# Kernel optimization log

Hardware: AMD Instinct MI355X
Metric: run time of the kernel (lower is better)

The kernel has to match this reference:

```python
import jax, jax.numpy as jnp
import numpy as np

BN_EPS = 1e-4  # KAIR BatchNorm2d eps


def conv1x1(x, W, b):
    # x: (b,c,h,w), W: (out,in), b: (out,)
    return jnp.einsum('oc,bchw->bohw', W, x) + b[None, :, None, None]


def setup_inputs() -> dict:
    key = jax.random.key(0)
    ks = jax.random.split(key, 16)
    b, c, h, w = 8, 64, 128, 128
    f32 = jnp.float32

    def rn(k, shape, s=0.05):
        return jax.random.normal(k, shape, f32) * s

    c3 = 3 * c
    return {
        'x': jax.random.normal(ks[0], (b, c, h, w), f32),
        'xf': jax.random.normal(ks[1], (b, c, h, w), f32),
        'xr': jax.random.normal(ks[2], (b, c, h, w), f32),
        'Wx': rn(ks[3], (c, c)), 'bx': jnp.zeros((c,), f32),
        'Wx1': rn(ks[4], (c, c)), 'bx1': jnp.zeros((c,), f32),
        'Wx2': rn(ks[5], (c, c)), 'bx2': jnp.zeros((c,), f32),
        'Wxf': rn(ks[6], (c, c)), 'bxf': jnp.zeros((c,), f32),
        'Wxr': rn(ks[7], (c, c)), 'bxr': jnp.zeros((c,), f32),
        'W_msa': rn(ks[8], (c3, c3, 3, 3)), 'b_msa': jnp.zeros((c3,), f32),
        'bn_gamma': jnp.ones((c3,), f32), 'bn_beta': jnp.zeros((c3,), f32),
        'bn_mean': jnp.zeros((c3,), f32), 'bn_var': jnp.ones((c3,), f32),
    }


def reference(x, xf, xr, Wx, bx, Wx1, bx1, Wx2, bx2, Wxf, bxf, Wxr, bxr,
              W_msa, b_msa, bn_gamma, bn_beta, bn_mean, bn_var):
    x_org = x
    # 1x1 conv projections (note: x1/x2 are projections of the projected x)
    xp = conv1x1(x, Wx, bx)
    x1 = conv1x1(xp, Wx1, bx1)
    x2 = conv1x1(xp, Wx2, bx2)
    xfp = conv1x1(xf, Wxf, bxf)
    xrp = conv1x1(xr, Wxr, bxr)

    # score1 = rearrange(x1,'b c h w->b h c w') @ rearrange(xf,'b c h w->b h w c') -> (b,h,c,c)
    score1 = jnp.einsum('bchw,bdhw->bhcd', x1, xfp)
    # feature_xf = score1 @ rearrange(x,'b c h w->b h c w'), rearranged back to (b,c,h,w)
    feature_xf = jnp.einsum('bhcd,bdhw->bchw', score1, xp)
    score2 = jnp.einsum('bchw,bdhw->bhcd', x2, xrp)
    feature_xr = jnp.einsum('bhcd,bdhw->bchw', score2, xp)

    out = jnp.concatenate([feature_xf, feature_xr, x_org], axis=1)  # (b,3c,h,w)
    # msa_conv: Conv2d(3c,3c,3,s=1,p=1) + BatchNorm2d(eval) + ReLU
    out = jax.lax.conv_general_dilated(
        out, W_msa, window_strides=(1, 1), padding='SAME',
        dimension_numbers=('NCHW', 'OIHW', 'NCHW'))
    out = out + b_msa[None, :, None, None]
    inv = jax.lax.rsqrt(bn_var + BN_EPS)
    out = (out - bn_mean[None, :, None, None]) * (bn_gamma * inv)[None, :, None, None] \
          + bn_beta[None, :, None, None]
    return jax.nn.relu(out)
```

## Files before the change

### kernel.cpp

```cpp
#include <hip/hip_runtime.h>

#define BATCH 8
#define C     64
#define H     128
#define WD    128
#define C3    192
#define HW    (H*WD)
#define PW    130
#define CBUF  (4*PW*64)

#define SWZ(r) ((((r) & 7) ^ (((r) >> 3) & 6)))

typedef __attribute__((ext_vector_type(8))) short short8;
typedef __attribute__((ext_vector_type(4))) float f32x4;
typedef unsigned short ushort_t;

__device__ __forceinline__ unsigned short f2bf(float f) {
    unsigned u = __builtin_bit_cast(unsigned, f);
    u += 0x7fffu + ((u >> 16) & 1u);
    return (unsigned short)(u >> 16);
}
__device__ __forceinline__ int pack2(unsigned short lo, unsigned short hi) {
    return (int)(((unsigned)hi << 16) | (unsigned)lo);
}

__global__ __launch_bounds__(64) void compose_kernel(
    const float* __restrict__ Wx,  const float* __restrict__ bx,
    const float* __restrict__ Wx1, const float* __restrict__ bx1,
    const float* __restrict__ Wx2, const float* __restrict__ bx2,
    const float* __restrict__ Wxf, const float* __restrict__ bxf,
    const float* __restrict__ Wxr, const float* __restrict__ bxr,
    ushort_t* __restrict__ Wall, float* __restrict__ ball)
{
    int o = blockIdx.x;
    int c = threadIdx.x;
    Wall[0*4096 + o*64 + c] = f2bf(Wx [o*64 + c]);
    Wall[3*4096 + o*64 + c] = f2bf(Wxf[o*64 + c]);
    Wall[4*4096 + o*64 + c] = f2bf(Wxr[o*64 + c]);
    float a1 = 0.f, a2 = 0.f;
    for (int k = 0; k < 64; ++k) {
        float wc = Wx[k*64 + c];
        a1 += Wx1[o*64 + k] * wc;
        a2 += Wx2[o*64 + k] * wc;
    }
    Wall[1*4096 + o*64 + c] = f2bf(a1);
    Wall[2*4096 + o*64 + c] = f2bf(a2);
    float t1 = Wx1[o*64 + c] * bx[c];
    float t2 = Wx2[o*64 + c] * bx[c];
    for (int off = 32; off; off >>= 1) {
        t1 += __shfl_down(t1, off);
        t2 += __shfl_down(t2, off);
    }
    if (c == 0) {
        ball[0*64 + o] = bx[o];
        ball[1*64 + o] = bx1[o] + t1;
        ball[2*64 + o] = bx2[o] + t2;
        ball[3*64 + o] = bxf[o];
        ball[4*64 + o] = bxr[o];
    }
}

__global__ __launch_bounds__(256) void prep_kernel(
    const float* __restrict__ x, const float* __restrict__ xf,
    const float* __restrict__ xr,
    ushort_t* __restrict__ xcl, ushort_t* __restrict__ feat,
    ushort_t* __restrict__ xfT, ushort_t* __restrict__ xrT)
{
    int b  = blockIdx.x / PW, py = blockIdx.x % PW;
    int t  = threadIdx.x;
    const size_t prow = ((size_t)b*PW + py)*PW;

    if (py == 0 || py == PW-1) {
        int4 z = make_int4(0,0,0,0);
        for (int j = t; j < PW*128/8; j += 256) ((int4*)(feat + prow*128))[j] = z;
        for (int j = t; j < PW*64/8;  j += 256) ((int4*)(xcl  + prow*64 ))[j] = z;
        return;
    }
    if (t < 48) {
        int4 z = make_int4(0,0,0,0);
        if (t < 32) {
            int side = t >> 4, seg = t & 15;
            *(int4*)(feat + (prow + (side ? PW-1 : 0))*128 + seg*8) = z;
        } else {
            int u = t - 32, side = u >> 3, seg = u & 7;
            *(int4*)(xcl + (prow + (side ? PW-1 : 0))*64 + seg*8) = z;
        }
    }
    __shared__ ushort_t sx[128*72];
    const int y = py - 1;

    for (int k = t; k < 64*128; k += 256) {
        int c = k >> 7, xx = k & 127;
        sx[xx*72 + c] = f2bf(x[((size_t)b*C + c)*HW + (size_t)y*WD + xx]);
    }
    __syncthreads();
    for (int j = t; j < 128*8; j += 256) {
        int xx = j >> 3, seg = j & 7;
        *(int4*)(xcl + (prow + xx + 1)*64 + seg*8) = *(const int4*)(sx + xx*72 + seg*8);
    }
    __syncthreads();
    for (int k = t; k < 64*128; k += 256) {
        int c = k >> 7, xx = k & 127;
        sx[xx*72 + c] = f2bf(xf[((size_t)b*C + c)*HW + (size_t)y*WD + xx]);
    }
    __syncthreads();
    for (int j = t; j < 128*8; j += 256) {
        int xx = j >> 3, seg = j & 7;
        *(int4*)(xfT + (((size_t)b*128 + y)*128 + xx)*64 + seg*8) = *(const int4*)(sx + xx*72 + seg*8);
    }
    __syncthreads();
    for (int k = t; k < 64*128; k += 256) {
        int c = k >> 7, xx = k & 127;
        sx[xx*72 + c] = f2bf(xr[((size_t)b*C + c)*HW + (size_t)y*WD + xx]);
    }
    __syncthreads();
    for (int j = t; j < 128*8; j += 256) {
        int xx = j >> 3, seg = j & 7;
        *(int4*)(xrT + (((size_t)b*128 + y)*128 + xx)*64 + seg*8) = *(const int4*)(sx + xx*72 + seg*8);
    }
}

__global__ __launch_bounds__(256, 3) void attn_mfma(
    const ushort_t* __restrict__ xcl, const ushort_t* __restrict__ xfT,
    const ushort_t* __restrict__ xrT,
    const ushort_t* __restrict__ Wall, const float* __restrict__ ball,
    ushort_t* __restrict__ feat)
{
    __shared__ ushort_t lds[6*4096];
    ushort_t* P = lds;
    ushort_t* Q = lds + 4096;
    ushort_t* U = lds + 2*4096;
    ushort_t* R = lds + 3*4096;
    ushort_t* V = lds + 4*4096;
    ushort_t* T = lds + 5*4096;

    const int t = threadIdx.x;
    const int wv = t >> 6, lane = t & 63, m = lane & 15, quad = lane >> 4;
    const int b = blockIdx.x >> 7, h = blockIdx.x & 127;
    const size_t rowbase = ((size_t)b*PW + h + 1)*PW;
    const ushort_t* xrow  = xcl + (rowbase + 1)*64;
    const ushort_t* xfrow = xfT + ((size_t)b*128 + h)*128*64;
    const ushort_t* xrrow = xrT + ((size_t)b*128 + h)*128*64;

    auto stageT = [&](const ushort_t* base, ushort_t* dst) {
#pragma unroll
        for (int it = 0; it < 2; ++it) {
            int slot = it*256 + t;
            int w = slot >> 3, seg = slot & 7;
            *(int4*)(dst + w*64 + ((seg ^ SWZ(w)) << 3)) =
                *(const int4*)(base + w*64 + seg*8);
        }
    };
    auto projB = [&](const ushort_t* src, const ushort_t* W, const float* bias,
                     ushort_t* dst) {
        int arow = wv*16 + m;
        int sa = SWZ(arow);
#pragma unroll
        for (int nt = 0; nt < 4; ++nt) {
            f32x4 acc = {0.f,0.f,0.f,0.f};
#pragma unroll
            for (int k = 0; k < 2; ++k) {
                short8 a  = *(const short8*)(src + arow*64 + (((4*k+quad) ^ sa) << 3));
                short8 bb = *(const short8*)(W   + (nt*16 + m)*64  + k*32 + quad*8);
                acc = __builtin_amdgcn_mfma_f32_16x16x32_bf16(a, bb, acc, 0,0,0);
            }
            float bo = bias[nt*16 + m];
            int o = nt*16 + m, w0 = wv*16 + quad*4;
            int base = o*64 + (((w0 >> 3) ^ SWZ(o)) << 3) + (w0 & 7);
            *(int*)(dst + base)     = pack2(f2bf(acc[0]+bo), f2bf(acc[1]+bo));
            *(int*)(dst + base + 2) = pack2(f2bf(acc[2]+bo), f2bf(acc[3]+bo));
        }
    };
    auto projA = [&](const ushort_t* src, const ushort_t* W, const float* bias,
                     ushort_t* dstT) {
        float b4[4];
#pragma unroll
        for (int r = 0; r < 4; ++r) b4[r] = bias[wv*16 + quad*4 + r];
#pragma unroll
        for (int nt = 0; nt < 4; ++nt) {
            f32x4 acc = {0.f,0.f,0.f,0.f};
            int brow = nt*16 + m;
            int sb = SWZ(brow);
#pragma unroll
            for (int k = 0; k < 2; ++k) {
                short8 a  = *(const short8*)(W   + (wv*16 + m)*64  + k*32 + quad*8);
                short8 bb = *(const short8*)(src + brow*64 + (((4*k+quad) ^ sb) << 3));
                acc = __builtin_amdgcn_mfma_f32_16x16x32_bf16(a, bb, acc, 0,0,0);
            }
            int w = nt*16 + m, o0 = wv*16 + quad*4;
            int base = w*64 + (((o0 >> 3) ^ SWZ(w)) << 3) + (o0 & 7);
            *(int*)(dstT + base)     = pack2(f2bf(acc[0]+b4[0]), f2bf(acc[1]+b4[1]));
            *(int*)(dstT + base + 2) = pack2(f2bf(acc[2]+b4[2]), f2bf(acc[3]+b4[3]));
        }
    };
    auto scoreStep = [&](const ushort_t* A, const ushort_t* B, f32x4* sc) {
        int arow = wv*16 + m;
        int sa = SWZ(arow);
#pragma unroll
        for (int nt = 0; nt < 4; ++nt) {
            int brow = nt*16 + m;
            int sb = SWZ(brow);
#pragma unroll
            for (int k = 0; k < 2; ++k) {
                short8 a  = *(const short8*)(A + arow*64 + (((4*k+quad) ^ sa) << 3));
                short8 bb = *(const short8*)(B + brow*64 + (((4*k+quad) ^ sb) << 3));
                sc[nt] = __builtin_amdgcn_mfma_f32_16x16x32_bf16(a, bb, sc[nt], 0,0,0);
            }
        }
    };
    auto scoreDump = [&](const f32x4* sc, ushort_t* dst) {
        int c0 = wv*16 + quad*4;
#pragma unroll
        for (int nt = 0; nt < 4; ++nt) {
            int d = nt*16 + m;
            int gd = d >> 3, dl = d & 7;
#pragma unroll
            for (int r = 0; r < 4; ++r) {
                int row = c0 + r;
                dst[row*64 + ((gd ^ SWZ(row)) << 3) + dl] = f2bf(sc[nt][r]);
            }
        }
    };
    auto featF = [&](const ushort_t* Sc, const ushort_t* XpT, ushort_t* stg) {
        int arow = wv*16 + m;
        int sa = SWZ(arow);
#pragma unroll
        for (int nt = 0; nt < 4; ++nt) {
            f32x4 acc = {0.f,0.f,0.f,0.f};
            int brow = nt*16 + m;
            int sb = SWZ(brow);
#pragma unroll
            for (int k = 0; k < 2; ++k) {
                short8 a  = *(const short8*)(Sc  + arow*64 + (((4*k+quad) ^ sa) << 3));
                short8 bb = *(const short8*)(XpT + brow*64 + (((4*k+quad) ^ sb) << 3));
                acc = __builtin_amdgcn_mfma_f32_16x16x32_bf16(a, bb, acc, 0,0,0);
            }
            int w = nt*16 + m, c0 = wv*16 + quad*4;
            int base = w*64 + (((c0 >> 3) ^ SWZ(w)) << 3) + (c0 & 7);
            *(int*)(stg + base)     = pack2(f2bf(acc[0]), f2bf(acc[1]));
            *(int*)(stg + base + 2) = pack2(f2bf(acc[2]), f2bf(acc[3]));
        }
    };
    auto emitPair = [&](const ushort_t* O1, const ushort_t* O2, int wc) {
#pragma unroll
        for (int it = 0; it < 4; ++it) {
            int j = (it & 1)*256 + t;
            const ushort_t* S = (it < 2) ? O1 : O2;
            int half = (it < 2) ? 0 : 64;
            int row = j >> 3, seg = j & 7;
            int4 v = *(const int4*)(S + row*64 + ((seg ^ SWZ(row)) << 3));
            *(int4*)(feat + (rowbase + wc + 1 + row)*128 + half + seg*8) = v;
        }
    };

    const ushort_t* W0 = Wall;            const float* b0 = ball;
    const ushort_t* W1 = Wall + 4096;     const float* b1 = ball + 64;
    const ushort_t* W2 = Wall + 2*4096;   const float* b2 = ball + 128;
    const ushort_t* W3 = Wall + 3*4096;   const float* b3 = ball + 192;
    const ushort_t* W4 = Wall + 4*4096;   const float* b4 = ball + 256;

    f32x4 sc1[4], sc2[4];
#pragma unroll
    for (int i = 0; i < 4; ++i) { sc1[i] = (f32x4){0,0,0,0}; sc2[i] = (f32x4){0,0,0,0}; }

    stageT(xrow, P); stageT(xfrow, Q); stageT(xrrow, U);
    __syncthreads();
    projB(P, W1, b1, R);  projB(P, W2, b2, V);  projB(Q, W3, b3, T);
    __syncthreads();
    scoreStep(R, T, sc1); projB(U, W4, b4, Q);
    __syncthreads();
    scoreStep(V, Q, sc2);
    stageT(xrow + 64*64, P); stageT(xfrow + 64*64, T); stageT(xrrow + 64*64, U);
    __syncthreads();
    projB(P, W1, b1, R);  projB(P, W2, b2, V);  projB(T, W3, b3, Q);
    __syncthreads();
    scoreStep(R, Q, sc1); projB(U, W4, b4, T);
    __syncthreads();
    scoreStep(V, T, sc2);
    stageT(xrow, P);
    __syncthreads();

    scoreDump(sc1, Q);  scoreDump(sc2, U);
    __syncthreads();
    projA(P, W0, b0, R);
    __syncthreads();
    featF(Q, R, P);  featF(U, R, T);  stageT(xrow + 64*64, V);
    __syncthreads();
    emitPair(P, T, 0);
    __syncthreads();
    projA(V, W0, b0, R);
    __syncthreads();
    featF(Q, R, V);  featF(U, R, T);
    __syncthreads();
    emitPair(V, T, 64);
}

__global__ __launch_bounds__(256) void pack_kernel(const float* __restrict__ W,
                                                   ushort_t* __restrict__ Wpk)
{
    int k = blockIdx.x*256 + threadIdx.x;
    if (k >= 12*54*64) return;
    int lane = k & 63, os = k >> 6;
    int otile = os / 54, s = os % 54;
    int tap = s / 6, icc = s % 6;
    int o   = otile*16 + (lane & 15);
    int ic0 = icc*32 + (lane >> 4)*8;
    ushort_t v[8];
#pragma unroll
    for (int j = 0; j < 8; ++j)
        v[j] = f2bf(W[(size_t)(o*C3 + ic0 + j)*9 + tap]);
    *(int4*)(Wpk + (size_t)k*8) = *(const int4*)v;
}

__global__ __launch_bounds__(512, 2) void conv_mfma(
    const ushort_t* __restrict__ feat, const ushort_t* __restrict__ xcl,
    const ushort_t* __restrict__ Wpk,
    const float* __restrict__ bias, const float* __restrict__ gamma,
    const float* __restrict__ beta, const float* __restrict__ mean,
    const float* __restrict__ var,  float* __restrict__ out)
{
    __shared__ ushort_t sA[2*CBUF];

    const int t = threadIdx.x;
    const int wv = t >> 6, lane = t & 63;
    const int m = lane & 15, quad = lane >> 4;
    const int b  = blockIdx.x >> 6, y0 = (blockIdx.x & 63)*2;
    const int yi = wv & 1, og = wv >> 1;

    f32x4 acc[32];
#pragma unroll
    for (int i = 0; i < 32; ++i) acc[i] = (f32x4){0.f,0.f,0.f,0.f};

    auto produce = [&](int ch, int bufi) {
        ushort_t* dst = sA + bufi*CBUF;
        const ushort_t* base = (ch < 2) ? feat : xcl;
        const int ps = (ch < 2) ? 128 : 64;
        const int co = (ch == 1) ? 64 : 0;
        const int pt = t - 384;
        for (int i = 0; i < 32; ++i) {
            int sl = i*128 + pt;
            int wi = sl & 7, rowgx = sl >> 3;
            int row = rowgx / PW, gx = rowgx - row*PW;
            int wl = wi ^ (gx & 7);
            const ushort_t* g = base + (((size_t)b*PW + y0 + row)*PW + gx)*ps
                                     + co + wl*8;
            __builtin_amdgcn_global_load_lds(
                (const __attribute__((address_space(1))) unsigned int*)g,
                (__attribute__((address_space(3))) unsigned int*)(dst + (size_t)sl*8),
                16, 0, 0);
        }
        if (pt < 64) {
            int sl = 4096 + pt;
            int wi = sl & 7, rowgx = sl >> 3;
            int row = rowgx / PW, gx = rowgx - row*PW;
            int wl = wi ^ (gx & 7);
            const ushort_t* g = base + (((size_t)b*PW + y0 + row)*PW + gx)*ps
                                     + co + wl*8;
            __builtin_amdgcn_global_load_lds(
                (const __attribute__((address_space(1))) unsigned int*)g,
                (__attribute__((address_space(3))) unsigned int*)(dst + (size_t)sl*8),
                16, 0, 0);
        }
    };

    auto compute = [&](int ch, int bufi) {
        const ushort_t* src = sA + bufi*CBUF;
        short8 bf[8], bfn[8];
#pragma unroll
        for (int j = 0; j < 4; ++j)
#pragma unroll
            for (int k = 0; k < 2; ++k)
                bf[j*2+k] = *(const short8*)(Wpk +
                    (((size_t)(og*4+j)*54 + ch*2 + k)*64 + lane)*8);
#pragma unroll
        for (int tap = 0; tap < 9; ++tap) {
            if (tap < 8) {
#pragma unroll
                for (int j = 0; j < 4; ++j)
#pragma unroll
                    for (int k = 0; k < 2; ++k)
                        bfn[j*2+k] = *(const short8*)(Wpk +
                            (((size_t)(og*4+j)*54 + (tap+1)*6 + ch*2 + k)*64 + lane)*8);
            }
            const int ky = tap/3, kx = tap - ky*3;
            const int sw = (kx + m) & 7;
            const int rowb = ((yi + ky)*PW + kx + m)*64;
            const int g0 = (quad ^ sw)*8, g1 = ((quad+4) ^ sw)*8;
#pragma unroll
            for (int xt = 0; xt < 8; ++xt) {
                short8 af0 = *(const short8*)(src + rowb + xt*1024 + g0);
                short8 af1 = *(const short8*)(src + rowb + xt*1024 + g1);
#pragma unroll
                for (int j = 0; j < 4; ++j) {
                    acc[j*8+xt] = __builtin_amdgcn_mfma_f32_16x16x32_bf16(af0, bf[j*2],   acc[j*8+xt], 0,0,0);
                    acc[j*8+xt] = __builtin_amdgcn_mfma_f32_16x16x32_bf16(af1, bf[j*2+1], acc[j*8+xt], 0,0,0);
                }
            }
#pragma unroll
            for (int q = 0; q < 8; ++q) bf[q] = bfn[q];
        }
    };

    if (wv >= 6) produce(0, 0);
    __syncthreads();
    for (int ch = 0; ch < 3; ++ch) {
        if (wv >= 6) { if (ch < 2) produce(ch + 1, (ch + 1) & 1); }
        else          compute(ch, ch & 1);
        __syncthreads();
    }

    float* sOut = (float*)sA;
    for (int y = 0; y < 2; ++y) {
        if (wv < 6 && yi == y) {
#pragma unroll
            for (int j = 0; j < 4; ++j) {
                int o = (og*4 + j)*16 + m;
                float A  = gamma[o] * rsqrtf(var[o] + 1e-4f);
                float Bv = (bias[o] - mean[o])*A + beta[o];
#pragma unroll
                for (int xt = 0; xt < 8; ++xt) {
                    f32x4 a4 = acc[j*8 + xt];
                    *(float4*)(sOut + o*132 + xt*16 + quad*4) =
                        make_float4(fmaxf(a4[0]*A + Bv, 0.f), fmaxf(a4[1]*A + Bv, 0.f),
                                    fmaxf(a4[2]*A + Bv, 0.f), fmaxf(a4[3]*A + Bv, 0.f));
                }
            }
        }
        __syncthreads();
#pragma unroll
        for (int i = 0; i < 12; ++i) {
            int s = i*512 + t;
            int o = s >> 5, xs4 = (s & 31)*4;
            float4 v = *(const float4*)(sOut + o*132 + xs4);
            *(float4*)(out + (((size_t)b*C3 + o)*H + y0 + y)*WD + xs4) = v;
        }
        __syncthreads();
    }
}

extern "C" void kernel_launch(void* const* d_in, const int* in_sizes, int n_in,
                              void* d_out, int out_size, void* d_ws, size_t ws_size,
                              hipStream_t stream)
{
    const float* x   = (const float*)d_in[0];
    const float* xf  = (const float*)d_in[1];
    const float* xr  = (const float*)d_in[2];
    const float* Wx  = (const float*)d_in[3];
    const float* bx  = (const float*)d_in[4];
    const float* Wx1 = (const float*)d_in[5];
    const float* bx1 = (const float*)d_in[6];
    const float* Wx2 = (const float*)d_in[7];
    const float* bx2 = (const float*)d_in[8];
    const float* Wxf = (const float*)d_in[9];
    const float* bxf = (const float*)d_in[10];
    const float* Wxr = (const float*)d_in[11];
    const float* bxr = (const float*)d_in[12];
    const float* Wm  = (const float*)d_in[13];
    const float* bms = (const float*)d_in[14];
    const float* gam = (const float*)d_in[15];
    const float* bet = (const float*)d_in[16];
    const float* mea = (const float*)d_in[17];
    const float* va  = (const float*)d_in[18];
    (void)in_sizes; (void)n_in; (void)out_size; (void)ws_size;

    ushort_t* feat = (ushort_t*)d_ws;
    ushort_t* xcl  = (ushort_t*)((char*)d_ws + 34611200);
    ushort_t* Wpk  = (ushort_t*)((char*)d_ws + 51916800);
    ushort_t* Wall = (ushort_t*)((char*)d_ws + 52700000);
    float*    ball = (float*)   ((char*)d_ws + 52750000);
    ushort_t* xfT  = (ushort_t*)d_out;
    ushort_t* xrT  = (ushort_t*)((char*)d_out + 16777216);
    float* outp = (float*)d_out;

    compose_kernel<<<dim3(64), dim3(64), 0, stream>>>(
        Wx, bx, Wx1, bx1, Wx2, bx2, Wxf, bxf, Wxr, bxr, Wall, ball);
    pack_kernel<<<dim3(162), dim3(256), 0, stream>>>(Wm, Wpk);
    prep_kernel<<<dim3(BATCH*PW), dim3(256), 0, stream>>>(
        x, xf, xr, xcl, feat, xfT, xrT);
    attn_mfma<<<dim3(BATCH*H), dim3(256), 0, stream>>>(
        xcl, xfT, xrT, Wall, ball, feat);
    conv_mfma<<<dim3(BATCH*64), dim3(512), 0, stream>>>(
        feat, xcl, Wpk, bms, gam, bet, mea, va, outp);
}
```

Measured before the change: 371.5 us.

## Use 16 waves per conv block, all loading and computing, instead of producer warps

The 3x3 conv kernel now runs 1024 threads per block. The old split had 6 compute waves and 2 dedicated producer waves; now all 16 waves both stage the next channel chunk asynchronously and compute. Each wave covers a smaller output tile (3 output tiles by 4 x-tiles) with fewer accumulators, and it loads weights per tap without double buffering. The aim is more waves to hide latency and no idle producers, at the cost of more redundant weight loads from global memory and more LDS A-fragment reads per MFMA.

```diff
diff --git a/kernel.cpp b/kernel.cpp
--- a/kernel.cpp
+++ b/kernel.cpp
@@ -312,7 +312,7 @@
     *(int4*)(Wpk + (size_t)k*8) = *(const int4*)v;
 }
 
-__global__ __launch_bounds__(512, 2) void conv_mfma(
+__global__ __launch_bounds__(1024, 4) void conv_mfma(
     const ushort_t* __restrict__ feat, const ushort_t* __restrict__ xcl,
     const ushort_t* __restrict__ Wpk,
     const float* __restrict__ bias, const float* __restrict__ gamma,
@@ -325,20 +325,22 @@
     const int wv = t >> 6, lane = t & 63;
     const int m = lane & 15, quad = lane >> 4;
     const int b  = blockIdx.x >> 6, y0 = (blockIdx.x & 63)*2;
-    const int yi = wv & 1, og = wv >> 1;
-
-    f32x4 acc[32];
-#pragma unroll
-    for (int i = 0; i < 32; ++i) acc[i] = (f32x4){0.f,0.f,0.f,0.f};
-
-    auto produce = [&](int ch, int bufi) {
+    const int yi = wv & 1;
+    const int xh = (wv >> 1) & 1;
+    const int oq = wv >> 2;
+
+    f32x4 acc[12];
+#pragma unroll
+    for (int i = 0; i < 12; ++i) acc[i] = (f32x4){0.f,0.f,0.f,0.f};
+
+    auto stageAll = [&](int ch, int bufi) {
         ushort_t* dst = sA + bufi*CBUF;
         const ushort_t* base = (ch < 2) ? feat : xcl;
         const int ps = (ch < 2) ? 128 : 64;
         const int co = (ch == 1) ? 64 : 0;
-        const int pt = t - 384;
-        for (int i = 0; i < 32; ++i) {
-            int sl = i*128 + pt;
+#pragma unroll
+        for (int i = 0; i < 4; ++i) {
+            int sl = i*1024 + t;
             int wi = sl & 7, rowgx = sl >> 3;
             int row = rowgx / PW, gx = rowgx - row*PW;
             int wl = wi ^ (gx & 7);
@@ -349,8 +351,8 @@
                 (__attribute__((address_space(3))) unsigned int*)(dst + (size_t)sl*8),
                 16, 0, 0);
         }
-        if (pt < 64) {
-            int sl = 4096 + pt;
+        if (t < 64) {
+            int sl = 4096 + t;
             int wi = sl & 7, rowgx = sl >> 3;
             int row = rowgx / PW, gx = rowgx - row*PW;
             int wl = wi ^ (gx & 7);
@@ -365,62 +367,53 @@
 
     auto compute = [&](int ch, int bufi) {
         const ushort_t* src = sA + bufi*CBUF;
-        short8 bf[8], bfn[8];
-#pragma unroll
-        for (int j = 0; j < 4; ++j)
-#pragma unroll
-            for (int k = 0; k < 2; ++k)
-                bf[j*2+k] = *(const short8*)(Wpk +
-                    (((size_t)(og*4+j)*54 + ch*2 + k)*64 + lane)*8);
 #pragma unroll
         for (int tap = 0; tap < 9; ++tap) {
-            if (tap < 8) {
-#pragma unroll
-                for (int j = 0; j < 4; ++j)
-#pragma unroll
-                    for (int k = 0; k < 2; ++k)
-                        bfn[j*2+k] = *(const short8*)(Wpk +
-                            (((size_t)(og*4+j)*54 + (tap+1)*6 + ch*2 + k)*64 + lane)*8);
-            }
+            short8 bf[6];
+#pragma unroll
+            for (int j = 0; j < 3; ++j)
+#pragma unroll
+                for (int k = 0; k < 2; ++k)
+                    bf[j*2+k] = *(const short8*)(Wpk +
+                        (((size_t)(oq*3+j)*54 + tap*6 + ch*2 + k)*64 + lane)*8);
             const int ky = tap/3, kx = tap - ky*3;
             const int sw = (kx + m) & 7;
             const int rowb = ((yi + ky)*PW + kx + m)*64;
             const int g0 = (quad ^ sw)*8, g1 = ((quad+4) ^ sw)*8;
 #pragma unroll
-            for (int xt = 0; xt < 8; ++xt) {
+            for (int xtl = 0; xtl < 4; ++xtl) {
+                const int xt = xh*4 + xtl;
                 short8 af0 = *(const short8*)(src + rowb + xt*1024 + g0);
                 short8 af1 = *(const short8*)(src + rowb + xt*1024 + g1);
 #pragma unroll
-                for (int j = 0; j < 4; ++j) {
-                    acc[j*8+xt] = __builtin_amdgcn_mfma_f32_16x16x32_bf16(af0, bf[j*2],   acc[j*8+xt], 0,0,0);
-                    acc[j*8+xt] = __builtin_amdgcn_mfma_f32_16x16x32_bf16(af1, bf[j*2+1], acc[j*8+xt], 0,0,0);
+                for (int j = 0; j < 3; ++j) {
+                    acc[j*4+xtl] = __builtin_amdgcn_mfma_f32_16x16x32_bf16(af0, bf[j*2],   acc[j*4+xtl], 0,0,0);
+                    acc[j*4+xtl] = __builtin_amdgcn_mfma_f32_16x16x32_bf16(af1, bf[j*2+1], acc[j*4+xtl], 0,0,0);
                 }
             }
-#pragma unroll
-            for (int q = 0; q < 8; ++q) bf[q] = bfn[q];
-        }
-    };
-
-    if (wv >= 6) produce(0, 0);
+        }
+    };
+
+    stageAll(0, 0);
     __syncthreads();
     for (int ch = 0; ch < 3; ++ch) {
-        if (wv >= 6) { if (ch < 2) produce(ch + 1, (ch + 1) & 1); }
-        else          compute(ch, ch & 1);
+        if (ch < 2) stageAll(ch + 1, (ch + 1) & 1);
+        compute(ch, ch & 1);
         __syncthreads();
     }
 
     float* sOut = (float*)sA;
     for (int y = 0; y < 2; ++y) {
-        if (wv < 6 && yi == y) {
-#pragma unroll
-            for (int j = 0; j < 4; ++j) {
-                int o = (og*4 + j)*16 + m;
+        if (yi == y) {
+#pragma unroll
+            for (int j = 0; j < 3; ++j) {
+                int o = (oq*3 + j)*16 + m;
                 float A  = gamma[o] * rsqrtf(var[o] + 1e-4f);
                 float Bv = (bias[o] - mean[o])*A + beta[o];
 #pragma unroll
-                for (int xt = 0; xt < 8; ++xt) {
-                    f32x4 a4 = acc[j*8 + xt];
-                    *(float4*)(sOut + o*132 + xt*16 + quad*4) =
+                for (int xtl = 0; xtl < 4; ++xtl) {
+                    f32x4 a4 = acc[j*4 + xtl];
+                    *(float4*)(sOut + o*132 + (xh*4 + xtl)*16 + quad*4) =
                         make_float4(fmaxf(a4[0]*A + Bv, 0.f), fmaxf(a4[1]*A + Bv, 0.f),
                                     fmaxf(a4[2]*A + Bv, 0.f), fmaxf(a4[3]*A + Bv, 0.f));
                 }
@@ -428,8 +421,8 @@
         }
         __syncthreads();
 #pragma unroll
-        for (int i = 0; i < 12; ++i) {
-            int s = i*512 + t;
+        for (int i = 0; i < 6; ++i) {
+            int s = i*1024 + t;
             int o = s >> 5, xs4 = (s & 31)*4;
             float4 v = *(const float4*)(sOut + o*132 + xs4);
             *(float4*)(out + (((size_t)b*C3 + o)*H + y0 + y)*WD + xs4) = v;
@@ -479,6 +472,6 @@
         x, xf, xr, xcl, feat, xfT, xrT);
     attn_mfma<<<dim3(BATCH*H), dim3(256), 0, stream>>>(
         xcl, xfT, xrT, Wall, ball, feat);
-    conv_mfma<<<dim3(BATCH*64), dim3(512), 0, stream>>>(
+    conv_mfma<<<dim3(BATCH*64), dim3(1024), 0, stream>>>(
         feat, xcl, Wpk, bms, gam, bet, mea, va, outp);
 }
```

Result: no change. 374.6 us (+0.8%).

## Split prep kernel per input and use all conv waves for compute

Applied to the files above, without the earlier changes.

The prep kernel now launches three times as many blocks, one slice per input tensor (x, xf, xr), instead of each block converting all three serially. This exposes more parallelism and drops the extra barriers between conversions. In the conv kernel the two dedicated producer waves are removed. All 8 waves now both issue the async global-to-LDS loads and compute, each holding 3 output-channel groups instead of 4, which lowers accumulator register use. The risk is that load issue is no longer decoupled from the MFMA work, so memory latency may be less well hidden.

```diff
diff --git a/kernel.cpp b/kernel.cpp
--- a/kernel.cpp
+++ b/kernel.cpp
@@ -66,57 +66,56 @@
     ushort_t* __restrict__ xcl, ushort_t* __restrict__ feat,
     ushort_t* __restrict__ xfT, ushort_t* __restrict__ xrT)
 {
-    int b  = blockIdx.x / PW, py = blockIdx.x % PW;
-    int t  = threadIdx.x;
+    const int which = blockIdx.x / (BATCH*PW);
+    const int r = blockIdx.x % (BATCH*PW);
+    const int b = r / PW, py = r % PW;
+    const int t = threadIdx.x;
     const size_t prow = ((size_t)b*PW + py)*PW;
 
-    if (py == 0 || py == PW-1) {
-        int4 z = make_int4(0,0,0,0);
-        for (int j = t; j < PW*128/8; j += 256) ((int4*)(feat + prow*128))[j] = z;
-        for (int j = t; j < PW*64/8;  j += 256) ((int4*)(xcl  + prow*64 ))[j] = z;
+    __shared__ ushort_t sx[128*72];
+
+    if (which == 0) {
+        if (py == 0 || py == PW-1) {
+            int4 z = make_int4(0,0,0,0);
+            for (int j = t; j < PW*128/8; j += 256) ((int4*)(feat + prow*128))[j] = z;
+            for (int j = t; j < PW*64/8;  j += 256) ((int4*)(xcl  + prow*64 ))[j] = z;
+            return;
+        }
+        if (t < 48) {
+            int4 z = make_int4(0,0,0,0);
+            if (t < 32) {
+                int side = t >> 4, seg = t & 15;
+                *(int4*)(feat + (prow + (side ? PW-1 : 0))*128 + seg*8) = z;
+            } else {
+                int u = t - 32, side = u >> 3, seg = u & 7;
+                *(int4*)(xcl + (prow + (side ? PW-1 : 0))*64 + seg*8) = z;
+            }
+        }
+        const int y = py - 1;
+        for (int k = t; k < 64*128; k += 256) {
+            int c = k >> 7, xx = k & 127;
+            sx[xx*72 + c] = f2bf(x[((size_t)b*C + c)*HW + (size_t)y*WD + xx]);
+        }
+        __syncthreads();
+        for (int j = t; j < 128*8; j += 256) {
+            int xx = j >> 3, seg = j & 7;
+            *(int4*)(xcl + (prow + xx + 1)*64 + seg*8) = *(const int4*)(sx + xx*72 + seg*8);
+        }
         return;
     }
-    if (t < 48) {
-        int4 z = make_int4(0,0,0,0);
-        if (t < 32) {
-            int side = t >> 4, seg = t & 15;
-            *(int4*)(feat + (prow + (side ? PW-1 : 0))*128 + seg*8) = z;
-        } else {
-            int u = t - 32, side = u >> 3, seg = u & 7;
-            *(int4*)(xcl + (prow + (side ? PW-1 : 0))*64 + seg*8) = z;
-        }
-    }
-    __shared__ ushort_t sx[128*72];
+
+    if (py == 0 || py == PW-1) return;
     const int y = py - 1;
-
+    const float* src = (which == 1) ? xf : xr;
+    ushort_t* dstT   = (which == 1) ? xfT : xrT;
     for (int k = t; k < 64*128; k += 256) {
         int c = k >> 7, xx = k & 127;
-        sx[xx*72 + c] = f2bf(x[((size_t)b*C + c)*HW + (size_t)y*WD + xx]);
+        sx[xx*72 + c] = f2bf(src[((size_t)b*C + c)*HW + (size_t)y*WD + xx]);
     }
     __syncthreads();
     for (int j = t; j < 128*8; j += 256) {
         int xx = j >> 3, seg = j & 7;
-        *(int4*)(xcl + (prow + xx + 1)*64 + seg*8) = *(const int4*)(sx + xx*72 + seg*8);
-    }
-    __syncthreads();
-    for (int k = t; k < 64*128; k += 256) {
-        int c = k >> 7, xx = k & 127;
-        sx[xx*72 + c] = f2bf(xf[((size_t)b*C + c)*HW + (size_t)y*WD + xx]);
-    }
-    __syncthreads();
-    for (int j = t; j < 128*8; j += 256) {
-        int xx = j >> 3, seg = j & 7;
-        *(int4*)(xfT + (((size_t)b*128 + y)*128 + xx)*64 + seg*8) = *(const int4*)(sx + xx*72 + seg*8);
-    }
-    __syncthreads();
-    for (int k = t; k < 64*128; k += 256) {
-        int c = k >> 7, xx = k & 127;
-        sx[xx*72 + c] = f2bf(xr[((size_t)b*C + c)*HW + (size_t)y*WD + xx]);
-    }
-    __syncthreads();
-    for (int j = t; j < 128*8; j += 256) {
-        int xx = j >> 3, seg = j & 7;
-        *(int4*)(xrT + (((size_t)b*128 + y)*128 + xx)*64 + seg*8) = *(const int4*)(sx + xx*72 + seg*8);
+        *(int4*)(dstT + (((size_t)b*128 + y)*128 + xx)*64 + seg*8) = *(const int4*)(sx + xx*72 + seg*8);
     }
 }
 
@@ -327,18 +326,18 @@
     const int b  = blockIdx.x >> 6, y0 = (blockIdx.x & 63)*2;
     const int yi = wv & 1, og = wv >> 1;
 
-    f32x4 acc[32];
-#pragma unroll
-    for (int i = 0; i < 32; ++i) acc[i] = (f32x4){0.f,0.f,0.f,0.f};
-
-    auto produce = [&](int ch, int bufi) {
+    f32x4 acc[24];
+#pragma unroll
+    for (int i = 0; i < 24; ++i) acc[i] = (f32x4){0.f,0.f,0.f,0.f};
+
+    auto stageAll = [&](int ch, int bufi) {
         ushort_t* dst = sA + bufi*CBUF;
         const ushort_t* base = (ch < 2) ? feat : xcl;
         const int ps = (ch < 2) ? 128 : 64;
         const int co = (ch == 1) ? 64 : 0;
-        const int pt = t - 384;
-        for (int i = 0; i < 32; ++i) {
-            int sl = i*128 + pt;
+#pragma unroll
+        for (int i = 0; i < 8; ++i) {
+            int sl = i*512 + t;
             int wi = sl & 7, rowgx = sl >> 3;
             int row = rowgx / PW, gx = rowgx - row*PW;
             int wl = wi ^ (gx & 7);
@@ -349,8 +348,8 @@
                 (__attribute__((address_space(3))) unsigned int*)(dst + (size_t)sl*8),
                 16, 0, 0);
         }
-        if (pt < 64) {
-            int sl = 4096 + pt;
+        if (t < 64) {
+            int sl = 4096 + t;
             int wi = sl & 7, rowgx = sl >> 3;
             int row = rowgx / PW, gx = rowgx - row*PW;
             int wl = wi ^ (gx & 7);
@@ -365,22 +364,22 @@
 
     auto compute = [&](int ch, int bufi) {
         const ushort_t* src = sA + bufi*CBUF;
-        short8 bf[8], bfn[8];
-#pragma unroll
-        for (int j = 0; j < 4; ++j)
+        short8 bf[6], bfn[6];
+#pragma unroll
+        for (int j = 0; j < 3; ++j)
 #pragma unroll
             for (int k = 0; k < 2; ++k)
                 bf[j*2+k] = *(const short8*)(Wpk +
-                    (((size_t)(og*4+j)*54 + ch*2 + k)*64 + lane)*8);
+                    (((size_t)(og*3+j)*54 + ch*2 + k)*64 + lane)*8);
 #pragma unroll
         for (int tap = 0; tap < 9; ++tap) {
             if (tap < 8) {
 #pragma unroll
-                for (int j = 0; j < 4; ++j)
+                for (int j = 0; j < 3; ++j)
 #pragma unroll
                     for (int k = 0; k < 2; ++k)
                         bfn[j*2+k] = *(const short8*)(Wpk +
-                            (((size_t)(og*4+j)*54 + (tap+1)*6 + ch*2 + k)*64 + lane)*8);
+                            (((size_t)(og*3+j)*54 + (tap+1)*6 + ch*2 + k)*64 + lane)*8);
             }
             const int ky = tap/3, kx = tap - ky*3;
             const int sw = (kx + m) & 7;
@@ -391,30 +390,30 @@
                 short8 af0 = *(const short8*)(src + rowb + xt*1024 + g0);
                 short8 af1 = *(const short8*)(src + rowb + xt*1024 + g1);
 #pragma unroll
-                for (int j = 0; j < 4; ++j) {
+                for (int j = 0; j < 3; ++j) {
                     acc[j*8+xt] = __builtin_amdgcn_mfma_f32_16x16x32_bf16(af0, bf[j*2],   acc[j*8+xt], 0,0,0);
                     acc[j*8+xt] = __builtin_amdgcn_mfma_f32_16x16x32_bf16(af1, bf[j*2+1], acc[j*8+xt], 0,0,0);
                 }
             }
 #pragma unroll
-            for (int q = 0; q < 8; ++q) bf[q] = bfn[q];
-        }
-    };
-
-    if (wv >= 6) produce(0, 0);
+            for (int q = 0; q < 6; ++q) bf[q] = bfn[q];
+        }
+    };
+
+    stageAll(0, 0);
     __syncthreads();
     for (int ch = 0; ch < 3; ++ch) {
-        if (wv >= 6) { if (ch < 2) produce(ch + 1, (ch + 1) & 1); }
-        else          compute(ch, ch & 1);
+        if (ch < 2) stageAll(ch + 1, (ch + 1) & 1);
+        compute(ch, ch & 1);
         __syncthreads();
     }
 
     float* sOut = (float*)sA;
     for (int y = 0; y < 2; ++y) {
-        if (wv < 6 && yi == y) {
-#pragma unroll
-            for (int j = 0; j < 4; ++j) {
-                int o = (og*4 + j)*16 + m;
+        if (yi == y) {
+#pragma unroll
+            for (int j = 0; j < 3; ++j) {
+                int o = (og*3 + j)*16 + m;
                 float A  = gamma[o] * rsqrtf(var[o] + 1e-4f);
                 float Bv = (bias[o] - mean[o])*A + beta[o];
 #pragma unroll
@@ -475,7 +474,7 @@
     compose_kernel<<<dim3(64), dim3(64), 0, stream>>>(
         Wx, bx, Wx1, bx1, Wx2, bx2, Wxf, bxf, Wxr, bxr, Wall, ball);
     pack_kernel<<<dim3(162), dim3(256), 0, stream>>>(Wm, Wpk);
-    prep_kernel<<<dim3(BATCH*PW), dim3(256), 0, stream>>>(
+    prep_kernel<<<dim3(3*BATCH*PW), dim3(256), 0, stream>>>(
         x, xf, xr, xcl, feat, xfT, xrT);
     attn_mfma<<<dim3(BATCH*H), dim3(256), 0, stream>>>(
         xcl, xfT, xrT, Wall, ball, feat);
```

Result: faster. 356.8 us (-4.0%).
